# Kernel tuning notes

Measured on AMD Instinct MI355X. Metric: run time of the kernel, lower is better.

Reference implementation:

```python
import jax, jax.numpy as jnp
import numpy as np

# DCT-III (a.k.a. IDCT), unnormalized, scaled to match the DREAMPlace kernel:
#   y_k = x_0 + 2 * sum_{n=1}^{N-1} x_n * cos(pi * n * (2k+1) / (2N))
# (the docstring's Re{1/2 x0 + sum xn e^{j pi n (2k+1)/(2N)}} scaled by 2).
# Computed in O(N log N) via a length-2N FFT:
#   y_k = Re{ sum_n c_n x_n e^{j pi n/(2N)} e^{2 pi j n k/(2N)} }
# which is 2N * ifft(pad(a, 2N)) evaluated at k = 0..N-1, with
#   a_n = c_n * x_n * exp(j pi n / (2N)),  c_0 = 1, c_{n>0} = 2.

def _idct_last_dim(x):
    N = x.shape[-1]
    n = jnp.arange(N)
    c = jnp.where(n == 0, 1.0, 2.0).astype(x.dtype)
    twiddle = jnp.exp(1j * (jnp.pi / (2 * N)) * n.astype(jnp.float32)).astype(jnp.complex64)
    a = (c * x).astype(jnp.complex64) * twiddle          # [.., N]
    y = jnp.fft.ifft(a, n=2 * N, axis=-1)                # [.., 2N]
    return (y.real[..., :N] * (2 * N)).astype(x.dtype)


def setup_inputs() -> dict:
    key = jax.random.key(0)
    x = jax.random.normal(key, (4096, 4096), dtype=jnp.float32)
    return {"x": x}


def reference(x) -> jnp.ndarray:
    return _idct_last_dim(x)
```

## Files before the change

### kernel.cpp

```cpp
#include <hip/hip_runtime.h>
#include <cstdint>


#define NN 4096
#define HH 2048
#define BM 128
#define BN 128
#define BK 128

typedef int i32x4 __attribute__((ext_vector_type(4)));
typedef int i32x2 __attribute__((ext_vector_type(2)));

__device__ __forceinline__ void async_copy16(void* lds_base, const void* gptr) {
    __builtin_amdgcn_global_load_lds(
        (const __attribute__((address_space(1))) unsigned int*)gptr,
        (__attribute__((address_space(3))) unsigned int*)lds_base,
        16, 0, 0);
}

__device__ __forceinline__ int pack4(int q0, int q1, int q2, int q3) {
    return (q0 & 255) | ((q1 & 255) << 8) | ((q2 & 255) << 16) | ((q3 & 255) << 24);
}

__global__ __launch_bounds__(256) void prep_i8(const float* __restrict__ x,
                                               signed char* __restrict__ Ae,
                                               signed char* __restrict__ Ao,
                                               signed char* __restrict__ CEm,
                                               signed char* __restrict__ COm,
                                               float* __restrict__ se,
                                               float* __restrict__ so) {
    const int b = blockIdx.x;
    const int t = threadIdx.x;
    const float s = 3.834951969714103e-4f;

    if (b < 4096) {
        __shared__ float wmaxe[4], wmaxo[4];
        const float* xr = x + (size_t)b * NN;
        float v[16];
#pragma unroll
        for (int j = 0; j < 4; ++j) {
            float4 f = ((const float4*)xr)[t * 4 + j];
            v[j * 4 + 0] = f.x; v[j * 4 + 1] = f.y;
            v[j * 4 + 2] = f.z; v[j * 4 + 3] = f.w;
        }
        float emax = 1e-30f, omax = 1e-30f;
#pragma unroll
        for (int i = 0; i < 8; ++i) {
            emax = fmaxf(emax, __builtin_fabsf(v[2 * i]));
            omax = fmaxf(omax, __builtin_fabsf(v[2 * i + 1]));
        }
#pragma unroll
        for (int m = 1; m < 64; m <<= 1) {
            emax = fmaxf(emax, __shfl_xor(emax, m));
            omax = fmaxf(omax, __shfl_xor(omax, m));
        }
        const int wv = t >> 6;
        if ((t & 63) == 0) { wmaxe[wv] = emax; wmaxo[wv] = omax; }
        __syncthreads();
        const float rmax_e = fmaxf(fmaxf(wmaxe[0], wmaxe[1]), fmaxf(wmaxe[2], wmaxe[3]));
        const float rmax_o = fmaxf(fmaxf(wmaxo[0], wmaxo[1]), fmaxf(wmaxo[2], wmaxo[3]));
        const float inv_e = 127.0f / rmax_e, inv_o = 127.0f / rmax_o;
        int qe[8], qo[8];
#pragma unroll
        for (int i = 0; i < 8; ++i) {
            qe[i] = (int)rintf(v[2 * i] * inv_e);
            qo[i] = (int)rintf(v[2 * i + 1] * inv_o);
        }
        i32x2 oe, oo;
        oe[0] = pack4(qe[0], qe[1], qe[2], qe[3]);
        oe[1] = pack4(qe[4], qe[5], qe[6], qe[7]);
        oo[0] = pack4(qo[0], qo[1], qo[2], qo[3]);
        oo[1] = pack4(qo[4], qo[5], qo[6], qo[7]);
        ((i32x2*)(Ae + (size_t)b * HH))[t] = oe;
        ((i32x2*)(Ao + (size_t)b * HH))[t] = oo;
        if (t == 0) {
            se[b] = rmax_e * (1.0f / 127.0f);
            so[b] = rmax_o * (1.0f / 127.0f);
        }
    } else if (b < 6144) {
        const int k = b - 4096;
        const int twok1 = 2 * k + 1;
        int q[8];
#pragma unroll
        for (int i = 0; i < 8; ++i) {
            int m = t * 8 + i;
            int p = (2 * m * twok1) & 16383;
            float w = (m == 0) ? 1.0f : 2.0f;
            q[i] = (int)rintf(w * __cosf((float)p * s) * 63.5f);
        }
        i32x2 o;
        o[0] = pack4(q[0], q[1], q[2], q[3]);
        o[1] = pack4(q[4], q[5], q[6], q[7]);
        ((i32x2*)(CEm + (size_t)k * HH))[t] = o;
    } else {
        const int k = b - 6144;
        const int twok1 = 2 * k + 1;
        int q[8];
#pragma unroll
        for (int i = 0; i < 8; ++i) {
            int m = t * 8 + i;
            int p = ((2 * m + 1) * twok1) & 16383;
            q[i] = (int)rintf(__cosf((float)p * s) * 127.0f);
        }
        i32x2 o;
        o[0] = pack4(q[0], q[1], q[2], q[3]);
        o[1] = pack4(q[4], q[5], q[6], q[7]);
        ((i32x2*)(COm + (size_t)k * HH))[t] = o;
    }
}

__global__ __launch_bounds__(256, 2) void idct_gemm2(const signed char* __restrict__ Ae,
                                                     const signed char* __restrict__ Ao,
                                                     const signed char* __restrict__ CEm,
                                                     const signed char* __restrict__ COm,
                                                     const float* __restrict__ se,
                                                     const float* __restrict__ so,
                                                     float* __restrict__ C) {
    __shared__ __align__(16) signed char sAe[BM * BK];
    __shared__ __align__(16) signed char sAo[BM * BK];
    __shared__ __align__(16) signed char sCE[BN * BK];
    __shared__ __align__(16) signed char sCO[BN * BK];

    const int tid  = threadIdx.x;
    const int wave = tid >> 6;
    const int lane = tid & 63;
    const int waveM = wave >> 1;
    const int waveN = wave & 1;

    const int lid = blockIdx.y * gridDim.x + blockIdx.x;
    const int q8  = lid & 7;
    const int jj  = lid >> 3;
    const int bx  = (q8 & 1) * 8 + (jj & 7);
    const int by  = (q8 >> 1) * 8 + (jj >> 3);

    const int rowBase = by * BM;
    const int colBase = bx * BN;

    i32x4 accE[4][4] = {};
    i32x4 accO[4][4] = {};

    const int srow  = lane >> 3;
    const int sgran = lane & 7;
    const int ggcol = (sgran ^ srow) * 16;
    const int rmod  = lane & 7;
    const int quad  = lane >> 4;

    for (int k0 = 0; k0 < HH; k0 += BK) {
#pragma unroll
        for (int j = 0; j < 4; ++j) {
            int ck = wave * 4 + j;
            int r  = ck * 8 + srow;
            size_t aoff = (size_t)(rowBase + r) * HH + k0 + ggcol;
            size_t boff = (size_t)(colBase + r) * HH + k0 + ggcol;
            async_copy16(&sAe[ck * 1024], Ae + aoff);
            async_copy16(&sAo[ck * 1024], Ao + aoff);
            async_copy16(&sCE[ck * 1024], CEm + boff);
            async_copy16(&sCO[ck * 1024], COm + boff);
        }
        __syncthreads();

#pragma unroll
        for (int kk = 0; kk < 2; ++kk) {
            const int poff = ((kk * 4 + quad) ^ rmod) * 16;
            {
                i32x4 af[4], bfr[4];
#pragma unroll
                for (int mi = 0; mi < 4; ++mi) {
                    int r = waveM * 64 + mi * 16 + (lane & 15);
                    af[mi] = *(const i32x4*)&sAe[r * BK + poff];
                }
#pragma unroll
                for (int ni = 0; ni < 4; ++ni) {
                    int r = waveN * 64 + ni * 16 + (lane & 15);
                    bfr[ni] = *(const i32x4*)&sCE[r * BK + poff];
                }
#pragma unroll
                for (int mi = 0; mi < 4; ++mi)
#pragma unroll
                    for (int ni = 0; ni < 4; ++ni)
                        accE[mi][ni] = __builtin_amdgcn_mfma_i32_16x16x64_i8(
                            af[mi], bfr[ni], accE[mi][ni], 0, 0, 0);
            }
            {
                i32x4 af[4], bfr[4];
#pragma unroll
                for (int mi = 0; mi < 4; ++mi) {
                    int r = waveM * 64 + mi * 16 + (lane & 15);
                    af[mi] = *(const i32x4*)&sAo[r * BK + poff];
                }
#pragma unroll
                for (int ni = 0; ni < 4; ++ni) {
                    int r = waveN * 64 + ni * 16 + (lane & 15);
                    bfr[ni] = *(const i32x4*)&sCO[r * BK + poff];
                }
#pragma unroll
                for (int mi = 0; mi < 4; ++mi)
#pragma unroll
                    for (int ni = 0; ni < 4; ++ni)
                        accO[mi][ni] = __builtin_amdgcn_mfma_i32_16x16x64_i8(
                            af[mi], bfr[ni], accO[mi][ni], 0, 0, 0);
            }
        }
        __syncthreads();
    }

    const float sB_s = 2.0f / 127.0f;
    const int mrow0 = rowBase + waveM * 64 + (lane >> 4) * 4;
    const int ncol0 = colBase + waveN * 64 + (lane & 15);
#pragma unroll
    for (int mi = 0; mi < 4; ++mi)
#pragma unroll
        for (int ni = 0; ni < 4; ++ni)
#pragma unroll
            for (int rg = 0; rg < 4; ++rg) {
                int rr = mrow0 + mi * 16 + rg;
                int cc = ncol0 + ni * 16;
                float e = (float)accE[mi][ni][rg] * (se[rr] * sB_s);
                float o = (float)accO[mi][ni][rg] * (so[rr] * sB_s);
                C[(size_t)rr * NN + cc] = e + o;
                C[(size_t)rr * NN + (NN - 1 - cc)] = e - o;
            }
}

__global__ __launch_bounds__(256) void idct_naive(const float* __restrict__ x,
                                                  float* __restrict__ out) {
    int row = blockIdx.x;
    __shared__ float sx[NN];
    for (int i = threadIdx.x; i < NN; i += 256) sx[i] = x[(size_t)row * NN + i];
    __syncthreads();
    const float s = 3.834951969714103e-4f;
    for (int k = threadIdx.x; k < NN; k += 256) {
        int twok1 = 2 * k + 1;
        float acc = sx[0];
        int p = 0;
        for (int n = 1; n < NN; ++n) {
            p += twok1; p &= 16383;
            acc += 2.0f * sx[n] * __cosf((float)p * s);
        }
        out[(size_t)row * NN + k] = acc;
    }
}

extern "C" void kernel_launch(void* const* d_in, const int* in_sizes, int n_in,
                              void* d_out, int out_size, void* d_ws, size_t ws_size,
                              hipStream_t stream) {
    const float* x = (const float*)d_in[0];
    float* out = (float*)d_out;

    const size_t eA = (size_t)NN * HH;
    const size_t eC = (size_t)HH * HH;
    const size_t need = 2 * eA + 2 * eC + 2 * NN * sizeof(float);

    if (ws_size >= need) {
        signed char* Ae = (signed char*)d_ws;
        signed char* Ao = Ae + eA;
        signed char* CEm = Ao + eA;
        signed char* COm = CEm + eC;
        float* se = (float*)(COm + eC);
        float* so = se + NN;

        prep_i8<<<8192, 256, 0, stream>>>(x, Ae, Ao, CEm, COm, se, so);

        dim3 grid(HH / BN, NN / BM);
        idct_gemm2<<<grid, 256, 0, stream>>>(Ae, Ao, CEm, COm, se, so, out);
    } else {
        idct_naive<<<NN, 256, 0, stream>>>(x, out);
    }
}
```

Measured before the change: 143.2 us.

## Use 32x32 int8 MFMA with even/odd wave split and LDS epilogue exchange

The GEMM now assigns two waves to the even-part product and two to the odd-part product, each covering the full 128 rows, and issues 32x32x32 int8 MFMAs instead of 16x16x64. The even and odd results are combined in an epilogue that passes the odd half through LDS, which adds extra barriers and LDS traffic. The prep kernel is also split into a table-generation kernel and an input-quantization kernel, adding one launch. The goal is fewer fragment loads per MFMA and higher MFMA throughput, at the cost of a more serialized epilogue.

```diff
diff --git a/kernel.cpp b/kernel.cpp
--- a/kernel.cpp
+++ b/kernel.cpp
@@ -8,8 +8,9 @@
 #define BN 128
 #define BK 128
 
-typedef int i32x4 __attribute__((ext_vector_type(4)));
-typedef int i32x2 __attribute__((ext_vector_type(2)));
+typedef int i32x4  __attribute__((ext_vector_type(4)));
+typedef int i32x2  __attribute__((ext_vector_type(2)));
+typedef int i32x16 __attribute__((ext_vector_type(16)));
 
 __device__ __forceinline__ void async_copy16(void* lds_base, const void* gptr) {
     __builtin_amdgcn_global_load_lds(
@@ -22,63 +23,13 @@
     return (q0 & 255) | ((q1 & 255) << 8) | ((q2 & 255) << 16) | ((q3 & 255) << 24);
 }
 
-__global__ __launch_bounds__(256) void prep_i8(const float* __restrict__ x,
-                                               signed char* __restrict__ Ae,
-                                               signed char* __restrict__ Ao,
-                                               signed char* __restrict__ CEm,
-                                               signed char* __restrict__ COm,
-                                               float* __restrict__ se,
-                                               float* __restrict__ so) {
+__global__ __launch_bounds__(256) void prep_tbl(signed char* __restrict__ CEm,
+                                                signed char* __restrict__ COm) {
     const int b = blockIdx.x;
     const int t = threadIdx.x;
     const float s = 3.834951969714103e-4f;
-
-    if (b < 4096) {
-        __shared__ float wmaxe[4], wmaxo[4];
-        const float* xr = x + (size_t)b * NN;
-        float v[16];
-#pragma unroll
-        for (int j = 0; j < 4; ++j) {
-            float4 f = ((const float4*)xr)[t * 4 + j];
-            v[j * 4 + 0] = f.x; v[j * 4 + 1] = f.y;
-            v[j * 4 + 2] = f.z; v[j * 4 + 3] = f.w;
-        }
-        float emax = 1e-30f, omax = 1e-30f;
-#pragma unroll
-        for (int i = 0; i < 8; ++i) {
-            emax = fmaxf(emax, __builtin_fabsf(v[2 * i]));
-            omax = fmaxf(omax, __builtin_fabsf(v[2 * i + 1]));
-        }
-#pragma unroll
-        for (int m = 1; m < 64; m <<= 1) {
-            emax = fmaxf(emax, __shfl_xor(emax, m));
-            omax = fmaxf(omax, __shfl_xor(omax, m));
-        }
-        const int wv = t >> 6;
-        if ((t & 63) == 0) { wmaxe[wv] = emax; wmaxo[wv] = omax; }
-        __syncthreads();
-        const float rmax_e = fmaxf(fmaxf(wmaxe[0], wmaxe[1]), fmaxf(wmaxe[2], wmaxe[3]));
-        const float rmax_o = fmaxf(fmaxf(wmaxo[0], wmaxo[1]), fmaxf(wmaxo[2], wmaxo[3]));
-        const float inv_e = 127.0f / rmax_e, inv_o = 127.0f / rmax_o;
-        int qe[8], qo[8];
-#pragma unroll
-        for (int i = 0; i < 8; ++i) {
-            qe[i] = (int)rintf(v[2 * i] * inv_e);
-            qo[i] = (int)rintf(v[2 * i + 1] * inv_o);
-        }
-        i32x2 oe, oo;
-        oe[0] = pack4(qe[0], qe[1], qe[2], qe[3]);
-        oe[1] = pack4(qe[4], qe[5], qe[6], qe[7]);
-        oo[0] = pack4(qo[0], qo[1], qo[2], qo[3]);
-        oo[1] = pack4(qo[4], qo[5], qo[6], qo[7]);
-        ((i32x2*)(Ae + (size_t)b * HH))[t] = oe;
-        ((i32x2*)(Ao + (size_t)b * HH))[t] = oo;
-        if (t == 0) {
-            se[b] = rmax_e * (1.0f / 127.0f);
-            so[b] = rmax_o * (1.0f / 127.0f);
-        }
-    } else if (b < 6144) {
-        const int k = b - 4096;
+    if (b < 2048) {
+        const int k = b;
         const int twok1 = 2 * k + 1;
         int q[8];
 #pragma unroll
@@ -93,7 +44,7 @@
         o[1] = pack4(q[4], q[5], q[6], q[7]);
         ((i32x2*)(CEm + (size_t)k * HH))[t] = o;
     } else {
-        const int k = b - 6144;
+        const int k = b - 2048;
         const int twok1 = 2 * k + 1;
         int q[8];
 #pragma unroll
@@ -109,7 +60,59 @@
     }
 }
 
-__global__ __launch_bounds__(256, 2) void idct_gemm2(const signed char* __restrict__ Ae,
+__global__ __launch_bounds__(256) void prep_x(const float* __restrict__ x,
+                                              signed char* __restrict__ Ae,
+                                              signed char* __restrict__ Ao,
+                                              float* __restrict__ se,
+                                              float* __restrict__ so) {
+    const int b = blockIdx.x;
+    const int t = threadIdx.x;
+    __shared__ float wmaxe[4], wmaxo[4];
+    const float* xr = x + (size_t)b * NN;
+    float v[16];
+#pragma unroll
+    for (int j = 0; j < 4; ++j) {
+        float4 f = ((const float4*)xr)[t * 4 + j];
+        v[j * 4 + 0] = f.x; v[j * 4 + 1] = f.y;
+        v[j * 4 + 2] = f.z; v[j * 4 + 3] = f.w;
+    }
+    float emax = 1e-30f, omax = 1e-30f;
+#pragma unroll
+    for (int i = 0; i < 8; ++i) {
+        emax = fmaxf(emax, __builtin_fabsf(v[2 * i]));
+        omax = fmaxf(omax, __builtin_fabsf(v[2 * i + 1]));
+    }
+#pragma unroll
+    for (int m = 1; m < 64; m <<= 1) {
+        emax = fmaxf(emax, __shfl_xor(emax, m));
+        omax = fmaxf(omax, __shfl_xor(omax, m));
+    }
+    const int wv = t >> 6;
+    if ((t & 63) == 0) { wmaxe[wv] = emax; wmaxo[wv] = omax; }
+    __syncthreads();
+    const float rmax_e = fmaxf(fmaxf(wmaxe[0], wmaxe[1]), fmaxf(wmaxe[2], wmaxe[3]));
+    const float rmax_o = fmaxf(fmaxf(wmaxo[0], wmaxo[1]), fmaxf(wmaxo[2], wmaxo[3]));
+    const float inv_e = 127.0f / rmax_e, inv_o = 127.0f / rmax_o;
+    int qe[8], qo[8];
+#pragma unroll
+    for (int i = 0; i < 8; ++i) {
+        qe[i] = (int)rintf(v[2 * i] * inv_e);
+        qo[i] = (int)rintf(v[2 * i + 1] * inv_o);
+    }
+    i32x2 oe, oo;
+    oe[0] = pack4(qe[0], qe[1], qe[2], qe[3]);
+    oe[1] = pack4(qe[4], qe[5], qe[6], qe[7]);
+    oo[0] = pack4(qo[0], qo[1], qo[2], qo[3]);
+    oo[1] = pack4(qo[4], qo[5], qo[6], qo[7]);
+    ((i32x2*)(Ae + (size_t)b * HH))[t] = oe;
+    ((i32x2*)(Ao + (size_t)b * HH))[t] = oo;
+    if (t == 0) {
+        se[b] = rmax_e * (1.0f / 127.0f);
+        so[b] = rmax_o * (1.0f / 127.0f);
+    }
+}
+
+__global__ __launch_bounds__(256, 2) void idct_gemm3(const signed char* __restrict__ Ae,
                                                      const signed char* __restrict__ Ao,
                                                      const signed char* __restrict__ CEm,
                                                      const signed char* __restrict__ COm,
@@ -124,8 +127,8 @@
     const int tid  = threadIdx.x;
     const int wave = tid >> 6;
     const int lane = tid & 63;
-    const int waveM = wave >> 1;
-    const int waveN = wave & 1;
+    const int wN = wave & 1;
+    const int wO = wave >> 1;
 
     const int lid = blockIdx.y * gridDim.x + blockIdx.x;
     const int q8  = lid & 7;
@@ -136,14 +139,14 @@
     const int rowBase = by * BM;
     const int colBase = bx * BN;
 
-    i32x4 accE[4][4] = {};
-    i32x4 accO[4][4] = {};
+    i32x16 acc[4][2] = {};
 
     const int srow  = lane >> 3;
     const int sgran = lane & 7;
     const int ggcol = (sgran ^ srow) * 16;
-    const int rmod  = lane & 7;
-    const int quad  = lane >> 4;
+
+    const signed char* gSA = wO ? sAo : sAe;
+    const signed char* gSB = wO ? sCO : sCE;
 
     for (int k0 = 0; k0 < HH; k0 += BK) {
 #pragma unroll
@@ -160,66 +163,67 @@
         __syncthreads();
 
 #pragma unroll
-        for (int kk = 0; kk < 2; ++kk) {
-            const int poff = ((kk * 4 + quad) ^ rmod) * 16;
-            {
-                i32x4 af[4], bfr[4];
-#pragma unroll
-                for (int mi = 0; mi < 4; ++mi) {
-                    int r = waveM * 64 + mi * 16 + (lane & 15);
-                    af[mi] = *(const i32x4*)&sAe[r * BK + poff];
-                }
-#pragma unroll
-                for (int ni = 0; ni < 4; ++ni) {
-                    int r = waveN * 64 + ni * 16 + (lane & 15);
-                    bfr[ni] = *(const i32x4*)&sCE[r * BK + poff];
-                }
-#pragma unroll
-                for (int mi = 0; mi < 4; ++mi)
-#pragma unroll
-                    for (int ni = 0; ni < 4; ++ni)
-                        accE[mi][ni] = __builtin_amdgcn_mfma_i32_16x16x64_i8(
-                            af[mi], bfr[ni], accE[mi][ni], 0, 0, 0);
+        for (int kk = 0; kk < 4; ++kk) {
+            const int poff = ((kk * 2 + (lane >> 5)) ^ (lane & 7)) * 16;
+            i32x4 af[4], bf[2];
+#pragma unroll
+            for (int mi = 0; mi < 4; ++mi)
+                af[mi] = *(const i32x4*)&gSA[(mi * 32 + (lane & 31)) * BK + poff];
+#pragma unroll
+            for (int ni = 0; ni < 2; ++ni)
+                bf[ni] = *(const i32x4*)&gSB[(wN * 64 + ni * 32 + (lane & 31)) * BK + poff];
+#pragma unroll
+            for (int mi = 0; mi < 4; ++mi)
+#pragma unroll
+                for (int ni = 0; ni < 2; ++ni)
+                    acc[mi][ni] = __builtin_amdgcn_mfma_i32_32x32x32_i8(
+                        af[mi], bf[ni], acc[mi][ni], 0, 0, 0);
+        }
+        __syncthreads();
+    }
+
+    const float sB_s = 2.0f / 127.0f;
+    float* xch = (float*)(wN == 0 ? (void*)sAe : (void*)sAo);
+
+#pragma unroll
+    for (int h = 0; h < 2; ++h) {
+        __syncthreads();
+        if (wO == 1) {
+#pragma unroll
+            for (int j = 0; j < 2; ++j) {
+                const int mi = 2 * h + j;
+#pragma unroll
+                for (int ni = 0; ni < 2; ++ni)
+#pragma unroll
+                    for (int rg = 0; rg < 16; ++rg) {
+                        int rl = mi * 32 + (rg & 3) + 8 * (rg >> 2) + 4 * (lane >> 5);
+                        int cl = ni * 32 + (lane & 31);
+                        xch[(rl - h * 64) * 64 + cl] =
+                            (float)acc[mi][ni][rg] * (so[rowBase + rl] * sB_s);
+                    }
             }
-            {
-                i32x4 af[4], bfr[4];
-#pragma unroll
-                for (int mi = 0; mi < 4; ++mi) {
-                    int r = waveM * 64 + mi * 16 + (lane & 15);
-                    af[mi] = *(const i32x4*)&sAo[r * BK + poff];
-                }
-#pragma unroll
-                for (int ni = 0; ni < 4; ++ni) {
-                    int r = waveN * 64 + ni * 16 + (lane & 15);
-                    bfr[ni] = *(const i32x4*)&sCO[r * BK + poff];
-                }
-#pragma unroll
-                for (int mi = 0; mi < 4; ++mi)
-#pragma unroll
-                    for (int ni = 0; ni < 4; ++ni)
-                        accO[mi][ni] = __builtin_amdgcn_mfma_i32_16x16x64_i8(
-                            af[mi], bfr[ni], accO[mi][ni], 0, 0, 0);
+        }
+        __syncthreads();
+        if (wO == 0) {
+#pragma unroll
+            for (int j = 0; j < 2; ++j) {
+                const int mi = 2 * h + j;
+#pragma unroll
+                for (int ni = 0; ni < 2; ++ni)
+#pragma unroll
+                    for (int rg = 0; rg < 16; ++rg) {
+                        int rl = mi * 32 + (rg & 3) + 8 * (rg >> 2) + 4 * (lane >> 5);
+                        int cl = ni * 32 + (lane & 31);
+                        float e = (float)acc[mi][ni][rg] * (se[rowBase + rl] * sB_s);
+                        float o = xch[(rl - h * 64) * 64 + cl];
+                        int rr = rowBase + rl;
+                        int cc = colBase + wN * 64 + cl;
+                        C[(size_t)rr * NN + cc] = e + o;
+                        C[(size_t)rr * NN + (NN - 1 - cc)] = e - o;
+                    }
             }
         }
-        __syncthreads();
-    }
-
-    const float sB_s = 2.0f / 127.0f;
-    const int mrow0 = rowBase + waveM * 64 + (lane >> 4) * 4;
-    const int ncol0 = colBase + waveN * 64 + (lane & 15);
-#pragma unroll
-    for (int mi = 0; mi < 4; ++mi)
-#pragma unroll
-        for (int ni = 0; ni < 4; ++ni)
-#pragma unroll
-            for (int rg = 0; rg < 4; ++rg) {
-                int rr = mrow0 + mi * 16 + rg;
-                int cc = ncol0 + ni * 16;
-                float e = (float)accE[mi][ni][rg] * (se[rr] * sB_s);
-                float o = (float)accO[mi][ni][rg] * (so[rr] * sB_s);
-                C[(size_t)rr * NN + cc] = e + o;
-                C[(size_t)rr * NN + (NN - 1 - cc)] = e - o;
-            }
+    }
 }
 
 __global__ __launch_bounds__(256) void idct_naive(const float* __restrict__ x,
@@ -259,10 +263,11 @@
         float* se = (float*)(COm + eC);
         float* so = se + NN;
 
-        prep_i8<<<8192, 256, 0, stream>>>(x, Ae, Ao, CEm, COm, se, so);
+        prep_tbl<<<4096, 256, 0, stream>>>(CEm, COm);
+        prep_x<<<4096, 256, 0, stream>>>(x, Ae, Ao, se, so);
 
         dim3 grid(HH / BN, NN / BM);
-        idct_gemm2<<<grid, 256, 0, stream>>>(Ae, Ao, CEm, COm, se, so, out);
+        idct_gemm3<<<grid, 256, 0, stream>>>(Ae, Ao, CEm, COm, se, so, out);
     } else {
         idct_naive<<<NN, 256, 0, stream>>>(x, out);
     }
```

New measurement: 151.7 us. +5.9%, slower.

## Split even/odd GEMMs across waves to cut LDS fragment reads

Applied to the files above, without the earlier changes.

Reassigns the four waves so two compute the even-part GEMM and two the odd-part GEMM, each over a 64x128 tile, instead of every wave computing both halves on a 64x64 tile. This reduces LDS fragment loads per MFMA, since each A fragment is reused across eight B fragments. The even and odd results must then be combined across waves, which is done through an LDS exchange buffer with a swizzle and extra barriers in the epilogue.

```diff
diff --git a/kernel.cpp b/kernel.cpp
--- a/kernel.cpp
+++ b/kernel.cpp
@@ -109,23 +109,24 @@
     }
 }
 
-__global__ __launch_bounds__(256, 2) void idct_gemm2(const signed char* __restrict__ Ae,
+__global__ __launch_bounds__(256, 2) void idct_gemm6(const signed char* __restrict__ Ae,
                                                      const signed char* __restrict__ Ao,
                                                      const signed char* __restrict__ CEm,
                                                      const signed char* __restrict__ COm,
                                                      const float* __restrict__ se,
                                                      const float* __restrict__ so,
                                                      float* __restrict__ C) {
-    __shared__ __align__(16) signed char sAe[BM * BK];
-    __shared__ __align__(16) signed char sAo[BM * BK];
-    __shared__ __align__(16) signed char sCE[BN * BK];
-    __shared__ __align__(16) signed char sCO[BN * BK];
+    __shared__ __align__(16) signed char lds[65536];
+    signed char* sAe = lds;
+    signed char* sAo = lds + 16384;
+    signed char* sCE = lds + 32768;
+    signed char* sCO = lds + 49152;
 
     const int tid  = threadIdx.x;
     const int wave = tid >> 6;
     const int lane = tid & 63;
-    const int waveM = wave >> 1;
-    const int waveN = wave & 1;
+    const int wB = wave >> 1;
+    const int wM = wave & 1;
 
     const int lid = blockIdx.y * gridDim.x + blockIdx.x;
     const int q8  = lid & 7;
@@ -136,14 +137,16 @@
     const int rowBase = by * BM;
     const int colBase = bx * BN;
 
-    i32x4 accE[4][4] = {};
-    i32x4 accO[4][4] = {};
+    i32x4 acc[4][8] = {};
 
     const int srow  = lane >> 3;
     const int sgran = lane & 7;
     const int ggcol = (sgran ^ srow) * 16;
     const int rmod  = lane & 7;
     const int quad  = lane >> 4;
+
+    const signed char* SA = wB ? sAo : sAe;
+    const signed char* SB = wB ? sCO : sCE;
 
     for (int k0 = 0; k0 < HH; k0 += BK) {
 #pragma unroll
@@ -162,61 +165,58 @@
 #pragma unroll
         for (int kk = 0; kk < 2; ++kk) {
             const int poff = ((kk * 4 + quad) ^ rmod) * 16;
-            {
-                i32x4 af[4], bfr[4];
-#pragma unroll
-                for (int mi = 0; mi < 4; ++mi) {
-                    int r = waveM * 64 + mi * 16 + (lane & 15);
-                    af[mi] = *(const i32x4*)&sAe[r * BK + poff];
-                }
-#pragma unroll
-                for (int ni = 0; ni < 4; ++ni) {
-                    int r = waveN * 64 + ni * 16 + (lane & 15);
-                    bfr[ni] = *(const i32x4*)&sCE[r * BK + poff];
-                }
+            i32x4 af[4];
+#pragma unroll
+            for (int mi = 0; mi < 4; ++mi) {
+                int r = wM * 64 + mi * 16 + (lane & 15);
+                af[mi] = *(const i32x4*)&SA[r * BK + poff];
+            }
+#pragma unroll
+            for (int ni = 0; ni < 8; ++ni) {
+                int r = ni * 16 + (lane & 15);
+                i32x4 bfr = *(const i32x4*)&SB[r * BK + poff];
 #pragma unroll
                 for (int mi = 0; mi < 4; ++mi)
-#pragma unroll
-                    for (int ni = 0; ni < 4; ++ni)
-                        accE[mi][ni] = __builtin_amdgcn_mfma_i32_16x16x64_i8(
-                            af[mi], bfr[ni], accE[mi][ni], 0, 0, 0);
-            }
-            {
-                i32x4 af[4], bfr[4];
-#pragma unroll
-                for (int mi = 0; mi < 4; ++mi) {
-                    int r = waveM * 64 + mi * 16 + (lane & 15);
-                    af[mi] = *(const i32x4*)&sAo[r * BK + poff];
-                }
-#pragma unroll
-                for (int ni = 0; ni < 4; ++ni) {
-                    int r = waveN * 64 + ni * 16 + (lane & 15);
-                    bfr[ni] = *(const i32x4*)&sCO[r * BK + poff];
-                }
-#pragma unroll
-                for (int mi = 0; mi < 4; ++mi)
-#pragma unroll
-                    for (int ni = 0; ni < 4; ++ni)
-                        accO[mi][ni] = __builtin_amdgcn_mfma_i32_16x16x64_i8(
-                            af[mi], bfr[ni], accO[mi][ni], 0, 0, 0);
+                    acc[mi][ni] = __builtin_amdgcn_mfma_i32_16x16x64_i8(
+                        af[mi], bfr, acc[mi][ni], 0, 0, 0);
             }
         }
         __syncthreads();
     }
 
     const float sB_s = 2.0f / 127.0f;
-    const int mrow0 = rowBase + waveM * 64 + (lane >> 4) * 4;
-    const int ncol0 = colBase + waveN * 64 + (lane & 15);
+    const float* scale = wB ? so : se;
+    float* xch = (float*)lds;
+
+    __syncthreads();
 #pragma unroll
     for (int mi = 0; mi < 4; ++mi)
 #pragma unroll
-        for (int ni = 0; ni < 4; ++ni)
+        for (int nj = 0; nj < 4; ++nj)
 #pragma unroll
             for (int rg = 0; rg < 4; ++rg) {
-                int rr = mrow0 + mi * 16 + rg;
-                int cc = ncol0 + ni * 16;
-                float e = (float)accE[mi][ni][rg] * (se[rr] * sB_s);
-                float o = (float)accO[mi][ni][rg] * (so[rr] * sB_s);
+                const int ni = wB ? nj : nj + 4;
+                int rl = wM * 64 + mi * 16 + (lane >> 4) * 4 + rg;
+                int cl = ni * 16 + (lane & 15);
+                float v = (float)acc[mi][ni][rg] * (scale[rowBase + rl] * sB_s);
+                xch[rl * 128 + (cl ^ (((rl >> 2) & 1) << 4))] = v;
+            }
+    __syncthreads();
+#pragma unroll
+    for (int mi = 0; mi < 4; ++mi)
+#pragma unroll
+        for (int nj = 0; nj < 4; ++nj)
+#pragma unroll
+            for (int rg = 0; rg < 4; ++rg) {
+                const int ni = wB ? nj + 4 : nj;
+                int rl = wM * 64 + mi * 16 + (lane >> 4) * 4 + rg;
+                int cl = ni * 16 + (lane & 15);
+                float own = (float)acc[mi][ni][rg] * (scale[rowBase + rl] * sB_s);
+                float oth = xch[rl * 128 + (cl ^ (((rl >> 2) & 1) << 4))];
+                float e = wB ? oth : own;
+                float o = wB ? own : oth;
+                int rr = rowBase + rl;
+                int cc = colBase + cl;
                 C[(size_t)rr * NN + cc] = e + o;
                 C[(size_t)rr * NN + (NN - 1 - cc)] = e - o;
             }
@@ -262,7 +262,7 @@
         prep_i8<<<8192, 256, 0, stream>>>(x, Ae, Ao, CEm, COm, se, so);
 
         dim3 grid(HH / BN, NN / BM);
-        idct_gemm2<<<grid, 256, 0, stream>>>(Ae, Ao, CEm, COm, se, so, out);
+        idct_gemm6<<<grid, 256, 0, stream>>>(Ae, Ao, CEm, COm, se, so, out);
     } else {
         idct_naive<<<NN, 256, 0, stream>>>(x, out);
     }
```

After: 145.9 us. Within noise of the previous version (+1.9%).
